# Kernel tuning notes

Hardware: AMD Instinct MI355X
Metric: run time of the kernel (lower is better)

## Reference

```python
import jax, jax.numpy as jnp
import numpy as np

B, L, H, NH = 8, 384, 512, 8
DH = H // NH
MAX_SEQ_LEN = 384


def setup_inputs() -> dict:
    key = jax.random.key(0)
    ks = jax.random.split(key, 16)
    s = 0.02
    seq_len = jnp.concatenate([
        jnp.array([L], dtype=jnp.int32),
        jax.random.randint(ks[3], (B - 1,), L // 2, L + 1, dtype=jnp.int32),
    ])
    return {
        "key": jax.random.normal(ks[0], (B, L, H), jnp.float32),
        "query": jax.random.normal(ks[1], (B, L, H), jnp.float32),
        "value": jax.random.normal(ks[2], (B, L, H), jnp.float32),
        "seq_len": seq_len,
        "pe": jax.random.normal(ks[4], (2 * MAX_SEQ_LEN + 1, H), jnp.float32) * s,
        "Wk": jax.random.normal(ks[5], (H, H), jnp.float32) * s,
        "bk": jnp.zeros((H,), jnp.float32),
        "Wq": jax.random.normal(ks[6], (H, H), jnp.float32) * s,
        "bq": jnp.zeros((H,), jnp.float32),
        "Wv": jax.random.normal(ks[7], (H, H), jnp.float32) * s,
        "bv": jnp.zeros((H,), jnp.float32),
        "Wr": jax.random.normal(ks[8], (H, H), jnp.float32) * s,
        "br": jnp.zeros((H,), jnp.float32),
        "u_bias": jax.random.normal(ks[9], (NH, DH), jnp.float32) * s,
        "v_bias": jax.random.normal(ks[10], (NH, DH), jnp.float32) * s,
        "Wff": jax.random.normal(ks[11], (H, H), jnp.float32) * s,
        "bff": jnp.zeros((H,), jnp.float32),
    }


def reference(key, query, value, seq_len, pe, Wk, bk, Wq, bq, Wv, bv, Wr, br, u_bias, v_bias, Wff, bff):
    # relative distances: rel[i, j] = j - i, in [-(L-1), L-1]
    rel = jnp.arange(L)[None, :] - jnp.arange(L)[:, None]          # [L, L]
    rpe = pe[rel + MAX_SEQ_LEN]                                    # [L, L, H]

    k = (key @ Wk.T + bk).reshape(B, L, NH, DH)
    q = (query @ Wq.T + bq).reshape(B, L, NH, DH)
    v = (value @ Wv.T + bv).reshape(B, L, NH, DH)
    rpe = (rpe @ Wr.T + br).reshape(L, L, NH, DH)

    # Transformer-XL score terms
    A = jnp.einsum('bihd,bjhd->bhij', q, k)                        # content-content
    Bt = jnp.einsum('bihd,ijhd->bhij', q, rpe)                     # content-position
    C = jnp.einsum('hd,bjhd->bhj', u_bias, k)[:, :, None, :]       # global content bias
    Dt = jnp.einsum('hd,ijhd->hij', v_bias, rpe)[None]             # global position bias

    scores = (A + Bt + C + Dt) / jnp.sqrt(jnp.float32(DH))
    key_mask = jnp.arange(L)[None, :] < seq_len[:, None]           # [B, L]
    scores = jnp.where(key_mask[:, None, None, :], scores, -1e15)
    attn = jax.nn.softmax(scores, axis=-1)                         # [B, NH, L, L]

    out = jnp.einsum('bhij,bjhd->bihd', attn, v).reshape(B, L, H)
    return out @ Wff.T + bff
```

## Files before the change

### kernel.cpp

```cpp
#include <hip/hip_runtime.h>

#define B_  8
#define L_  384
#define H_  512
#define NH_ 8
#define DH_ 64
#define RRM 768

typedef short bf16x8 __attribute__((ext_vector_type(8)));
typedef float f32x4  __attribute__((ext_vector_type(4)));
typedef unsigned int u32;
typedef u32 u32x4 __attribute__((ext_vector_type(4)));
#define MFMA_BF16 __builtin_amdgcn_mfma_f32_16x16x32_bf16

static __device__ __forceinline__ unsigned short f2bf(float f) {
    unsigned u = __builtin_bit_cast(unsigned, f);
    u += 0x7fffu + ((u >> 16) & 1u);
    return (unsigned short)(u >> 16);
}
static __device__ __forceinline__ float bf2f(unsigned short s) {
    unsigned u = ((unsigned)s) << 16;
    return __builtin_bit_cast(float, u);
}
static __device__ __forceinline__ u32 pk2(float lo, float hi) {
    u32 r;
    asm("v_cvt_pk_bf16_f32 %0, %1, %2" : "=v"(r) : "v"(lo), "v"(hi));
    return r;
}

template <bool IS_FF>
__global__ __launch_bounds__(256) void gemm_nt(
    const float* __restrict__ A0, const float* __restrict__ A1,
    const float* __restrict__ A2, const float* __restrict__ A3,
    const unsigned short* __restrict__ Abf,
    const float* __restrict__ W0, const float* __restrict__ W1,
    const float* __restrict__ W2, const float* __restrict__ W3,
    const float* __restrict__ W4,
    const float* __restrict__ b0, const float* __restrict__ b1,
    const float* __restrict__ b2, const float* __restrict__ b3,
    const float* __restrict__ b4,
    const float* __restrict__ ub, const float* __restrict__ vbias,
    unsigned short* __restrict__ qu, unsigned short* __restrict__ qv,
    unsigned short* __restrict__ kb, unsigned short* __restrict__ vT,
    unsigned short* __restrict__ rp, float* __restrict__ ff) {

    const int z = IS_FF ? 4 : blockIdx.z;
    if (!IS_FF && z == 3 && blockIdx.y >= 12) return;
    const float* Af   = z == 0 ? A0 : z == 1 ? A1 : z == 2 ? A2 : A3;
    const float* W    = z == 0 ? W0 : z == 1 ? W1 : z == 2 ? W2 : z == 3 ? W3 : W4;
    const float* bias = z == 0 ? b0 : z == 1 ? b1 : z == 2 ? b2 : z == 3 ? b3 : b4;

    __shared__ __align__(16) unsigned short AsF[2 * 64 * 64];
    __shared__ __align__(16) unsigned short BsF[2 * 128 * 64];

    const int tid = threadIdx.x;
    const int w = tid >> 6, lane = tid & 63;
    const int quad = lane >> 4, lm = lane & 15;
    const int wr = (w & 1) * 32;
    const int wc = (w >> 1) * 64;

    const int sr = lane >> 3, sj = lane & 7;
    const size_t aoff = (size_t)(blockIdx.y * 64 + w * 16 + sr) * 512 + sj * 8;
    const size_t boff = (size_t)(blockIdx.x * 128 + w * 32 + sr) * 512 + sj * 8;

    f32x4 la[2][2], lb[4][2];
    bf16x8 lah[2];

    auto LOAD = [&](int kc) {
        #pragma unroll
        for (int t = 0; t < 2; ++t) {
            if constexpr (IS_FF) {
                lah[t] = *(const bf16x8*)(Abf + aoff + t * 8 * 512 + kc * 64);
            } else {
                const float* p = Af + aoff + t * 8 * 512 + kc * 64;
                la[t][0] = *(const f32x4*)p;
                la[t][1] = *(const f32x4*)(p + 4);
            }
        }
        #pragma unroll
        for (int t = 0; t < 4; ++t) {
            const float* q = W + boff + t * 8 * 512 + kc * 64;
            lb[t][0] = *(const f32x4*)q;
            lb[t][1] = *(const f32x4*)(q + 4);
        }
    };
    auto WRITE = [&](int buf) {
        #pragma unroll
        for (int t = 0; t < 2; ++t) {
            const int off = buf * 4096 + (w * 16 + t * 8 + sr) * 64 + (sj ^ sr) * 8;
            if constexpr (IS_FF) {
                *(bf16x8*)&AsF[off] = lah[t];
            } else {
                u32x4 pa;
                pa[0] = pk2(la[t][0][0], la[t][0][1]);
                pa[1] = pk2(la[t][0][2], la[t][0][3]);
                pa[2] = pk2(la[t][1][0], la[t][1][1]);
                pa[3] = pk2(la[t][1][2], la[t][1][3]);
                *(u32x4*)&AsF[off] = pa;
            }
        }
        #pragma unroll
        for (int t = 0; t < 4; ++t) {
            const int off = buf * 8192 + (w * 32 + t * 8 + sr) * 64 + (sj ^ sr) * 8;
            u32x4 pb;
            pb[0] = pk2(lb[t][0][0], lb[t][0][1]);
            pb[1] = pk2(lb[t][0][2], lb[t][0][3]);
            pb[2] = pk2(lb[t][1][0], lb[t][1][1]);
            pb[3] = pk2(lb[t][1][2], lb[t][1][3]);
            *(u32x4*)&BsF[off] = pb;
        }
    };

    f32x4 acc[2][4] = {};
    LOAD(0);
    for (int kc = 0; kc < 8; ++kc) {
        const int buf = kc & 1;
        WRITE(buf);
        if (kc < 7) LOAD(kc + 1);
        __syncthreads();
        const int ba = buf * 4096, bb = buf * 8192;
        #pragma unroll
        for (int ks = 0; ks < 2; ++ks) {
            const int s = (((ks * 4 + quad) ^ (lm & 7))) * 8;
            bf16x8 a0 = *(const bf16x8*)&AsF[ba + (wr + lm) * 64 + s];
            bf16x8 a1 = *(const bf16x8*)&AsF[ba + (wr + 16 + lm) * 64 + s];
            bf16x8 w0 = *(const bf16x8*)&BsF[bb + (wc + lm) * 64 + s];
            bf16x8 w1 = *(const bf16x8*)&BsF[bb + (wc + 16 + lm) * 64 + s];
            bf16x8 w2 = *(const bf16x8*)&BsF[bb + (wc + 32 + lm) * 64 + s];
            bf16x8 w3 = *(const bf16x8*)&BsF[bb + (wc + 48 + lm) * 64 + s];
            acc[0][0] = MFMA_BF16(a0, w0, acc[0][0], 0, 0, 0);
            acc[0][1] = MFMA_BF16(a0, w1, acc[0][1], 0, 0, 0);
            acc[0][2] = MFMA_BF16(a0, w2, acc[0][2], 0, 0, 0);
            acc[0][3] = MFMA_BF16(a0, w3, acc[0][3], 0, 0, 0);
            acc[1][0] = MFMA_BF16(a1, w0, acc[1][0], 0, 0, 0);
            acc[1][1] = MFMA_BF16(a1, w1, acc[1][1], 0, 0, 0);
            acc[1][2] = MFMA_BF16(a1, w2, acc[1][2], 0, 0, 0);
            acc[1][3] = MFMA_BF16(a1, w3, acc[1][3], 0, 0, 0);
        }
        __syncthreads();
    }

    #pragma unroll
    for (int si = 0; si < 2; ++si) {
        #pragma unroll
        for (int sj2 = 0; sj2 < 4; ++sj2) {
            #pragma unroll
            for (int reg = 0; reg < 4; ++reg) {
                const int r = blockIdx.y * 64 + wr + si * 16 + quad * 4 + reg;
                const int c = blockIdx.x * 128 + wc + sj2 * 16 + lm;
                const float val = acc[si][sj2][reg] + bias[c];
                if (IS_FF) {
                    ff[r * 512 + c] = val;
                } else if (z == 0) {
                    const int bb2 = r / L_, ii = r - bb2 * L_;
                    const int h = c >> 6, d = c & 63;
                    const int idx = ((bb2 * NH_ + h) * L_ + ii) * DH_ + d;
                    qu[idx] = f2bf((val + ub[c]) * 0.125f);
                    qv[idx] = f2bf((val + vbias[c]) * 0.125f);
                } else if (z == 1) {
                    const int bb2 = r / L_, ii = r - bb2 * L_;
                    const int h = c >> 6, d = c & 63;
                    kb[((bb2 * NH_ + h) * L_ + ii) * DH_ + d] = f2bf(val);
                } else if (z == 2) {
                    const int bb2 = r / L_, ii = r - bb2 * L_;
                    const int h = c >> 6, d = c & 63;
                    vT[((bb2 * NH_ + h) * DH_ + d) * L_ + ii] = f2bf(val);
                } else {
                    rp[r * 512 + c] = f2bf(val);
                }
            }
        }
    }
}

#define BTSTR 424
__global__ __launch_bounds__(256) void attn_fused(
    const unsigned short* __restrict__ qu, const unsigned short* __restrict__ qv,
    const unsigned short* __restrict__ kbf, const unsigned short* __restrict__ vT,
    const unsigned short* __restrict__ rp, const int* __restrict__ seq_len,
    unsigned short* __restrict__ Obf) {
    __shared__ __align__(16) unsigned short BtP[32 * BTSTR];
    __shared__ float mx_red[32][2];
    __shared__ float sm_red[32][2];
    const int lane = threadIdx.x & 63, wv = threadIdx.x >> 6;
    const int quad = lane >> 4, lm = lane & 15;
    const int bh = blockIdx.y, b = bh >> 3, h = bh & 7;
    const int i0 = blockIdx.x * 32;
    const int sl = seq_len[b];
    const int msub = wv & 1, nh = wv >> 1;
    const int m_lo = 353 - i0;
    const int i_fr = i0 + msub * 16 + lm;

    {
        const unsigned short* qvr = qv + (size_t)(bh * L_ + i_fr) * DH_;
        const bf16x8 av0 = *(const bf16x8*)(qvr + quad * 8);
        const bf16x8 av1 = *(const bf16x8*)(qvr + 32 + quad * 8);
        #pragma unroll
        for (int ns = 0; ns < 13; ++ns) {
            const int ntl = nh * 208 + ns * 16;
            if (ntl <= sl + 30) {
                const int n = ntl + lm;
                const unsigned short* rrow = rp + (size_t)(m_lo + n) * 512 + h * 64;
                f32x4 bacc = {};
                bacc = MFMA_BF16(av0, *(const bf16x8*)(rrow + quad * 8), bacc, 0, 0, 0);
                bacc = MFMA_BF16(av1, *(const bf16x8*)(rrow + 32 + quad * 8), bacc, 0, 0, 0);
                #pragma unroll
                for (int reg = 0; reg < 4; ++reg) {
                    const int il = msub * 16 + quad * 4 + reg;
                    BtP[il * BTSTR + n] = f2bf(bacc[reg]);
                }
            }
        }
    }
    const unsigned short* qur = qu + (size_t)(bh * L_ + i_fr) * DH_;
    const bf16x8 au0 = *(const bf16x8*)(qur + quad * 8);
    const bf16x8 au1 = *(const bf16x8*)(qur + 32 + quad * 8);
    __syncthreads();

    f32x4 sc[12];
    #pragma unroll
    for (int ns = 0; ns < 12; ++ns) {
        const int jt = nh * 192 + ns * 16;
        if (jt < sl) {
            const unsigned short* krow = kbf + (size_t)(bh * L_ + jt + lm) * DH_;
            f32x4 a = {};
            a = MFMA_BF16(au0, *(const bf16x8*)(krow + quad * 8), a, 0, 0, 0);
            a = MFMA_BF16(au1, *(const bf16x8*)(krow + 32 + quad * 8), a, 0, 0, 0);
            sc[ns] = a;
        } else {
            sc[ns] = f32x4{-1e30f, -1e30f, -1e30f, -1e30f};
        }
    }
    const int jbase = nh * 192 + lm;
    #pragma unroll
    for (int ns = 0; ns < 12; ++ns) {
        const int j = jbase + ns * 16;
        #pragma unroll
        for (int reg = 0; reg < 4; ++reg) {
            const int il = msub * 16 + quad * 4 + reg;
            float val = -1e30f;
            if (j < sl) val = sc[ns][reg] + bf2f(BtP[il * BTSTR + (j - il + 31)]);
            sc[ns][reg] = val;
        }
    }

    const int il0 = msub * 16 + quad * 4;
    float mx4[4], sm4[4], inv4[4];
    #pragma unroll
    for (int reg = 0; reg < 4; ++reg) {
        float m = sc[0][reg];
        #pragma unroll
        for (int ns = 1; ns < 12; ++ns) m = fmaxf(m, sc[ns][reg]);
        #pragma unroll
        for (int o = 1; o < 16; o <<= 1) m = fmaxf(m, __shfl_xor(m, o));
        mx4[reg] = m;
    }
    if (lm == 0) {
        #pragma unroll
        for (int reg = 0; reg < 4; ++reg) mx_red[il0 + reg][nh] = mx4[reg];
    }
    __syncthreads();
    #pragma unroll
    for (int reg = 0; reg < 4; ++reg)
        mx4[reg] = fmaxf(mx_red[il0 + reg][0], mx_red[il0 + reg][1]);
    #pragma unroll
    for (int reg = 0; reg < 4; ++reg) sm4[reg] = 0.f;
    #pragma unroll
    for (int ns = 0; ns < 12; ++ns) {
        #pragma unroll
        for (int reg = 0; reg < 4; ++reg) {
            const float e = __expf(sc[ns][reg] - mx4[reg]);
            sc[ns][reg] = e;
            sm4[reg] += e;
        }
    }
    #pragma unroll
    for (int reg = 0; reg < 4; ++reg) {
        float s = sm4[reg];
        #pragma unroll
        for (int o = 1; o < 16; o <<= 1) s += __shfl_xor(s, o);
        sm4[reg] = s;
    }
    if (lm == 0) {
        #pragma unroll
        for (int reg = 0; reg < 4; ++reg) sm_red[il0 + reg][nh] = sm4[reg];
    }
    __syncthreads();
    #pragma unroll
    for (int reg = 0; reg < 4; ++reg)
        inv4[reg] = 1.f / (sm_red[il0 + reg][0] + sm_red[il0 + reg][1]);

    #pragma unroll
    for (int ns = 0; ns < 12; ++ns) {
        const int j = jbase + ns * 16;
        #pragma unroll
        for (int reg = 0; reg < 4; ++reg)
            BtP[(il0 + reg) * BTSTR + j] = f2bf(sc[ns][reg] * inv4[reg]);
    }
    __syncthreads();

    {
        const int pr = msub * 16 + lm;
        const int nkc = (sl + 31) >> 5;
        f32x4 oacc[2] = {};
        for (int kc = 0; kc < nkc; ++kc) {
            const bf16x8 af = *(const bf16x8*)&BtP[pr * BTSTR + kc * 32 + quad * 8];
            #pragma unroll
            for (int t = 0; t < 2; ++t) {
                const int n = nh * 32 + t * 16 + lm;
                const unsigned short* vrow = vT + (size_t)(bh * DH_ + n) * L_ + kc * 32 + quad * 8;
                oacc[t] = MFMA_BF16(af, *(const bf16x8*)(vrow), oacc[t], 0, 0, 0);
            }
        }
        #pragma unroll
        for (int t = 0; t < 2; ++t) {
            #pragma unroll
            for (int reg = 0; reg < 4; ++reg) {
                const int i = i0 + msub * 16 + quad * 4 + reg;
                const int d = nh * 32 + t * 16 + lm;
                Obf[(size_t)(b * L_ + i) * H_ + h * DH_ + d] = f2bf(oacc[t][reg]);
            }
        }
    }
}

extern "C" void kernel_launch(void* const* d_in, const int* in_sizes, int n_in,
                              void* d_out, int out_size, void* d_ws, size_t ws_size,
                              hipStream_t stream) {
    const float* key    = (const float*)d_in[0];
    const float* query  = (const float*)d_in[1];
    const float* value  = (const float*)d_in[2];
    const int*   seqlen = (const int*)d_in[3];
    const float* pe     = (const float*)d_in[4];
    const float* Wk     = (const float*)d_in[5];
    const float* bk     = (const float*)d_in[6];
    const float* Wq     = (const float*)d_in[7];
    const float* bq     = (const float*)d_in[8];
    const float* Wv     = (const float*)d_in[9];
    const float* bv     = (const float*)d_in[10];
    const float* Wr     = (const float*)d_in[11];
    const float* br     = (const float*)d_in[12];
    const float* u_bias = (const float*)d_in[13];
    const float* v_bias = (const float*)d_in[14];
    const float* Wff    = (const float*)d_in[15];
    const float* bff    = (const float*)d_in[16];

    const size_t nTok = (size_t)B_ * L_ * H_;
    const size_t nPe  = (size_t)RRM * H_;
    unsigned short* p  = (unsigned short*)d_ws;
    unsigned short* qu   = p; p += nTok;
    unsigned short* qv   = p; p += nTok;
    unsigned short* kb   = p; p += nTok;
    unsigned short* vT   = p; p += nTok;
    unsigned short* rp   = p; p += nPe + 512;
    unsigned short* Obf  = p; p += nTok;

    gemm_nt<false><<<dim3(4, 48, 4), 256, 0, stream>>>(
         query, key, value, pe,  nullptr,
         Wq, Wk, Wv, Wr, nullptr,
         bq, bk, bv, br, nullptr,
         u_bias, v_bias,
         qu, qv, kb, vT, rp,
         nullptr);

    attn_fused<<<dim3(L_ / 32, B_ * NH_), 256, 0, stream>>>(
        qu, qv, kb, vT, rp, seqlen, Obf);

    gemm_nt<true><<<dim3(4, 48, 1), 256, 0, stream>>>(
         nullptr, nullptr, nullptr, nullptr,  Obf,
         nullptr, nullptr, nullptr, nullptr, Wff,
         nullptr, nullptr, nullptr, nullptr, bff,
         nullptr, nullptr,
         nullptr, nullptr, nullptr, nullptr, nullptr,
         (float*)d_out);
}
```

Baseline: 155.8 us.

## Pre-convert weights to swizzled bf16 and stage B tiles via direct global-to-LDS loads

Adds a small kernel that converts all five weight matrices to bf16 once per call, already in the XOR-swizzled layout the GEMM's shared-memory tiles expect. The GEMMs then load B tiles with global_load_lds straight into LDS, skipping the per-block fp32 loads, register conversion and LDS writes. This halves weight read traffic inside the GEMMs and frees registers. The cost is an extra kernel launch and an extra pass over the weights, which is small relative to the GEMM work.

```diff
diff --git a/kernel.cpp b/kernel.cpp
--- a/kernel.cpp
+++ b/kernel.cpp
@@ -27,15 +27,39 @@
     asm("v_cvt_pk_bf16_f32 %0, %1, %2" : "=v"(r) : "v"(lo), "v"(hi));
     return r;
 }
+static __device__ __forceinline__ void glds16(const void* g, void* l) {
+    __builtin_amdgcn_global_load_lds(
+        (const __attribute__((address_space(1))) u32*)g,
+        (__attribute__((address_space(3))) u32*)l, 16, 0, 0);
+}
+
+struct WCvtArgs { const float* src[5]; unsigned short* dst[5]; };
+__global__ __launch_bounds__(256) void cvt_w(WCvtArgs a) {
+    const int gid = blockIdx.x * 256 + threadIdx.x;
+    const int m = gid >> 15;
+    const int rem = gid & 32767;
+    const int row = rem >> 6, c = rem & 63;
+    const int kc = c >> 3, sjd = c & 7;
+    const int sjs = sjd ^ (row & 7);
+    const float* s = a.src[m] + row * 512 + kc * 64 + sjs * 8;
+    const f32x4 v0 = *(const f32x4*)s;
+    const f32x4 v1 = *(const f32x4*)(s + 4);
+    u32x4 o;
+    o[0] = pk2(v0[0], v0[1]);
+    o[1] = pk2(v0[2], v0[3]);
+    o[2] = pk2(v1[0], v1[1]);
+    o[3] = pk2(v1[2], v1[3]);
+    *(u32x4*)(a.dst[m] + row * 512 + kc * 64 + sjd * 8) = o;
+}
 
 template <bool IS_FF>
 __global__ __launch_bounds__(256) void gemm_nt(
     const float* __restrict__ A0, const float* __restrict__ A1,
     const float* __restrict__ A2, const float* __restrict__ A3,
     const unsigned short* __restrict__ Abf,
-    const float* __restrict__ W0, const float* __restrict__ W1,
-    const float* __restrict__ W2, const float* __restrict__ W3,
-    const float* __restrict__ W4,
+    const unsigned short* __restrict__ W0, const unsigned short* __restrict__ W1,
+    const unsigned short* __restrict__ W2, const unsigned short* __restrict__ W3,
+    const unsigned short* __restrict__ W4,
     const float* __restrict__ b0, const float* __restrict__ b1,
     const float* __restrict__ b2, const float* __restrict__ b3,
     const float* __restrict__ b4,
@@ -47,7 +71,8 @@
     const int z = IS_FF ? 4 : blockIdx.z;
     if (!IS_FF && z == 3 && blockIdx.y >= 12) return;
     const float* Af   = z == 0 ? A0 : z == 1 ? A1 : z == 2 ? A2 : A3;
-    const float* W    = z == 0 ? W0 : z == 1 ? W1 : z == 2 ? W2 : z == 3 ? W3 : W4;
+    const unsigned short* Wb =
+        z == 0 ? W0 : z == 1 ? W1 : z == 2 ? W2 : z == 3 ? W3 : W4;
     const float* bias = z == 0 ? b0 : z == 1 ? b1 : z == 2 ? b2 : z == 3 ? b3 : b4;
 
     __shared__ __align__(16) unsigned short AsF[2 * 64 * 64];
@@ -61,12 +86,13 @@
 
     const int sr = lane >> 3, sj = lane & 7;
     const size_t aoff = (size_t)(blockIdx.y * 64 + w * 16 + sr) * 512 + sj * 8;
-    const size_t boff = (size_t)(blockIdx.x * 128 + w * 32 + sr) * 512 + sj * 8;
-
-    f32x4 la[2][2], lb[4][2];
+    const unsigned short* gB =
+        Wb + (size_t)(blockIdx.x * 128 + w * 32 + sr) * 512 + sj * 8;
+
+    f32x4 la[2][2];
     bf16x8 lah[2];
 
-    auto LOAD = [&](int kc) {
+    auto LOAD_A = [&](int kc) {
         #pragma unroll
         for (int t = 0; t < 2; ++t) {
             if constexpr (IS_FF) {
@@ -77,14 +103,8 @@
                 la[t][1] = *(const f32x4*)(p + 4);
             }
         }
-        #pragma unroll
-        for (int t = 0; t < 4; ++t) {
-            const float* q = W + boff + t * 8 * 512 + kc * 64;
-            lb[t][0] = *(const f32x4*)q;
-            lb[t][1] = *(const f32x4*)(q + 4);
-        }
     };
-    auto WRITE = [&](int buf) {
+    auto WRITE_A = [&](int buf) {
         #pragma unroll
         for (int t = 0; t < 2; ++t) {
             const int off = buf * 4096 + (w * 16 + t * 8 + sr) * 64 + (sj ^ sr) * 8;
@@ -99,24 +119,23 @@
                 *(u32x4*)&AsF[off] = pa;
             }
         }
+    };
+    auto STAGE_B = [&](int kc, int buf) {
         #pragma unroll
         for (int t = 0; t < 4; ++t) {
-            const int off = buf * 8192 + (w * 32 + t * 8 + sr) * 64 + (sj ^ sr) * 8;
-            u32x4 pb;
-            pb[0] = pk2(lb[t][0][0], lb[t][0][1]);
-            pb[1] = pk2(lb[t][0][2], lb[t][0][3]);
-            pb[2] = pk2(lb[t][1][0], lb[t][1][1]);
-            pb[3] = pk2(lb[t][1][2], lb[t][1][3]);
-            *(u32x4*)&BsF[off] = pb;
+            int off = buf * 8192 + (w * 32 + t * 8) * 64;
+            off = __builtin_amdgcn_readfirstlane(off);
+            glds16(gB + t * 8 * 512 + kc * 64, &BsF[off]);
         }
     };
 
     f32x4 acc[2][4] = {};
-    LOAD(0);
+    LOAD_A(0);
     for (int kc = 0; kc < 8; ++kc) {
         const int buf = kc & 1;
-        WRITE(buf);
-        if (kc < 7) LOAD(kc + 1);
+        WRITE_A(buf);
+        STAGE_B(kc, buf);
+        if (kc < 7) LOAD_A(kc + 1);
         __syncthreads();
         const int ba = buf * 4096, bb = buf * 8192;
         #pragma unroll
@@ -347,6 +366,7 @@
 
     const size_t nTok = (size_t)B_ * L_ * H_;
     const size_t nPe  = (size_t)RRM * H_;
+    const size_t nW   = (size_t)H_ * H_;
     unsigned short* p  = (unsigned short*)d_ws;
     unsigned short* qu   = p; p += nTok;
     unsigned short* qv   = p; p += nTok;
@@ -354,10 +374,23 @@
     unsigned short* vT   = p; p += nTok;
     unsigned short* rp   = p; p += nPe + 512;
     unsigned short* Obf  = p; p += nTok;
+    unsigned short* Wqb  = p; p += nW;
+    unsigned short* Wkb  = p; p += nW;
+    unsigned short* Wvb  = p; p += nW;
+    unsigned short* Wrb  = p; p += nW;
+    unsigned short* Wffb = p; p += nW;
+
+    WCvtArgs wa;
+    wa.src[0] = Wq;  wa.dst[0] = Wqb;
+    wa.src[1] = Wk;  wa.dst[1] = Wkb;
+    wa.src[2] = Wv;  wa.dst[2] = Wvb;
+    wa.src[3] = Wr;  wa.dst[3] = Wrb;
+    wa.src[4] = Wff; wa.dst[4] = Wffb;
+    cvt_w<<<640, 256, 0, stream>>>(wa);
 
     gemm_nt<false><<<dim3(4, 48, 4), 256, 0, stream>>>(
          query, key, value, pe,  nullptr,
-         Wq, Wk, Wv, Wr, nullptr,
+         Wqb, Wkb, Wvb, Wrb, nullptr,
          bq, bk, bv, br, nullptr,
          u_bias, v_bias,
          qu, qv, kb, vT, rp,
@@ -368,7 +401,7 @@
 
     gemm_nt<true><<<dim3(4, 48, 1), 256, 0, stream>>>(
          nullptr, nullptr, nullptr, nullptr,  Obf,
-         nullptr, nullptr, nullptr, nullptr, Wff,
+         nullptr, nullptr, nullptr, nullptr, Wffb,
          nullptr, nullptr, nullptr, nullptr, bff,
          nullptr, nullptr,
          nullptr, nullptr, nullptr, nullptr, nullptr,
```

New measurement: 152.3 us. 1.02x faster.
